# Performance work log

Measured on AMD Instinct MI355X. Metric: run time of the kernel, lower is better.

The kernel has to match this reference:

```python
import jax, jax.numpy as jnp
import numpy as np

N = 8192
DIM_IN = 256
DIM_Q = 64
DIM_K = 64
E = 262144


def setup_inputs() -> dict:
    key = jax.random.key(0)
    ks = jax.random.split(key, 8)
    x = jax.random.normal(ks[0], (N, DIM_IN), dtype=jnp.float32)
    edge_index = jax.random.randint(ks[1], (2, E), 0, N, dtype=jnp.int64)
    s_in = 1.0 / np.sqrt(DIM_IN)
    Wq = jax.random.normal(ks[2], (DIM_IN, DIM_Q), dtype=jnp.float32) * s_in
    bq = jnp.zeros((DIM_Q,), dtype=jnp.float32)
    Wk = jax.random.normal(ks[3], (DIM_IN, DIM_K), dtype=jnp.float32) * s_in
    bk = jnp.zeros((DIM_K,), dtype=jnp.float32)
    Wv = jax.random.normal(ks[4], (DIM_IN, DIM_K), dtype=jnp.float32) * s_in
    bv = jnp.zeros((DIM_K,), dtype=jnp.float32)
    return {"x": x, "edge_index": edge_index, "Wq": Wq, "bq": bq,
            "Wk": Wk, "bk": bk, "Wv": Wv, "bv": bv}


def reference(x, edge_index, Wq, bq, Wk, bk, Wv, bv):
    # q/k/v projections (Dense layers)
    q = x @ Wq + bq            # (N, dim_q)
    k = x @ Wk + bk            # (N, dim_k)
    v = x @ Wv + bv            # (N, dim_k)
    n = x.shape[0]
    # scatter-built dense adjacency, as in the original module
    adj = jnp.zeros((n, n), dtype=x.dtype).at[edge_index[0], edge_index[1]].set(1.0)
    scale = 1.0 / jnp.sqrt(jnp.asarray(q.shape[-1], dtype=x.dtype))
    a = (q @ k.T) * scale      # (N, N)
    a = a * adj + (1.0 - adj) * (-1000000.0)
    attn = jax.nn.softmax(a, axis=-1)
    return attn @ v            # (N, dim_k)
```

## Files before the change

### kernel.cpp

```cpp
#include <hip/hip_runtime.h>
#include <hip/hip_bf16.h>

#define NROW 8192
#define DIM_IN 256
#define DIMK 64
#define NDIM 192
#define NEDGE 262144
#define CAP 128

using bf16 = __hip_bfloat16;
typedef _Float16 f16;
typedef _Float16 f16x8 __attribute__((ext_vector_type(8)));
typedef _Float16 f16x4 __attribute__((ext_vector_type(4)));
typedef float f32x4 __attribute__((ext_vector_type(4)));
typedef unsigned short u16x8 __attribute__((ext_vector_type(8)));

__device__ __forceinline__ float b2f(bf16 x) { return __bfloat162float(x); }
__device__ __forceinline__ float us2f(unsigned short u) {
    return __uint_as_float(((unsigned)u) << 16);
}
__device__ __forceinline__ void wave_sync() {
    asm volatile("s_waitcnt lgkmcnt(0)" ::: "memory");
    __builtin_amdgcn_sched_barrier(0);
}

__device__ __forceinline__ int probe_isb(const unsigned short* xw, int lane) {
    int ex = (xw[lane] >> 7) & 0xFF;
    unsigned long long b = __ballot(ex >= 100 && ex <= 140);
    return (__popcll(b) >= 56) ? 1 : 0;
}
__device__ __forceinline__ int probe_is64(const int* ei, int lane) {
    unsigned long long b = __ballot(ei[2 * lane + 1] != 0);
    return (b == 0ULL) ? 1 : 0;
}
__device__ __forceinline__ int src_at(const int* p, int e, int is64) {
    return is64 ? p[2 * e] : p[e];
}
__device__ __forceinline__ int dst_at(const int* p, int e, int is64) {
    return is64 ? p[2 * (NEDGE + e)] : p[NEDGE + e];
}

__device__ __forceinline__ f16x8 ldcvt(const void* x, size_t off, int isb) {
    f16x8 r;
    if (isb) {
        u16x8 u = *(const u16x8*)((const unsigned short*)x + off);
        #pragma unroll
        for (int i = 0; i < 8; ++i) r[i] = (f16)us2f(u[i]);
    } else {
        float4 f0 = *(const float4*)((const float*)x + off);
        float4 f1 = *(const float4*)((const float*)x + off + 4);
        r[0] = (f16)f0.x; r[1] = (f16)f0.y; r[2] = (f16)f0.z; r[3] = (f16)f0.w;
        r[4] = (f16)f1.x; r[5] = (f16)f1.y; r[6] = (f16)f1.z; r[7] = (f16)f1.w;
    }
    return r;
}

__device__ __forceinline__ void proj_tile16(
    const void* x, const f16* wt, const void* bq, const void* bk,
    const void* bv, int isb, int r0, int wave, int lane,
    f16* qh, f16* kh, f16* vh)
{
    int n0 = wave * 48;
    int lr = lane & 15;
    int lk = (lane >> 4) * 8;

    f32x4 acc0 = {0.f, 0.f, 0.f, 0.f}, acc1 = acc0, acc2 = acc0;
    size_t abase = (size_t)(r0 + lr) * DIM_IN + lk;
    const f16* bp = wt + (size_t)(n0 + lr) * DIM_IN + lk;

    #pragma unroll
    for (int ks = 0; ks < 8; ++ks) {
        f16x8 a  = ldcvt(x, abase + ks * 32, isb);
        f16x8 b0 = *(const f16x8*)(bp + ks * 32);
        f16x8 b1 = *(const f16x8*)(bp + 16 * DIM_IN + ks * 32);
        f16x8 b2 = *(const f16x8*)(bp + 32 * DIM_IN + ks * 32);
        acc0 = __builtin_amdgcn_mfma_f32_16x16x32_f16(a, b0, acc0, 0, 0, 0);
        acc1 = __builtin_amdgcn_mfma_f32_16x16x32_f16(a, b1, acc1, 0, 0, 0);
        acc2 = __builtin_amdgcn_mfma_f32_16x16x32_f16(a, b2, acc2, 0, 0, 0);
    }

    #pragma unroll
    for (int tt = 0; tt < 3; ++tt) {
        f32x4 a = (tt == 0) ? acc0 : (tt == 1) ? acc1 : acc2;
        int d = n0 + tt * 16 + lr;
        int mat = d >> 6, dd = d & 63;
        const void* bb = (mat == 0) ? bq : (mat == 1) ? bk : bv;
        float bias = isb ? b2f(((const bf16*)bb)[dd]) : ((const float*)bb)[dd];
        f16* o = (mat == 0) ? qh : (mat == 1) ? kh : vh;
        #pragma unroll
        for (int j = 0; j < 4; ++j) {
            int r = r0 + (lane >> 4) * 4 + j;
            o[(size_t)r * DIMK + dd] = (f16)(a[j] + bias);
        }
    }
}

__device__ __forceinline__ void attn_row(
    const f16* qh, const f16* kh, const f16* vh, const int* cursor,
    const unsigned short* bucket, float* out, int row, int lane,
    unsigned* bm, unsigned short* nb, float* sc)
{
    *(uint4*)(bm + 4 * lane) = make_uint4(0u, 0u, 0u, 0u);
    wave_sync();

    int deg = cursor[row];
    if (deg > CAP) deg = CAP;
    const unsigned short* bk_ = bucket + (size_t)row * CAP;
    for (int e = lane; e < deg; e += 64) {
        int j = bk_[e];
        atomicOr(&bm[j >> 5], 1u << (j & 31));
    }
    wave_sync();

    uint4 wv = *(const uint4*)(bm + 4 * lane);
    int pc = __popc(wv.x) + __popc(wv.y) + __popc(wv.z) + __popc(wv.w);
    int incl = pc;
    #pragma unroll
    for (int o = 1; o < 64; o <<= 1) {
        int n = __shfl_up(incl, o);
        if (lane >= o) incl += n;
    }
    int nn = __shfl(incl, 63);
    int idx = incl - pc;
    unsigned wrds[4] = {wv.x, wv.y, wv.z, wv.w};
    #pragma unroll
    for (int wi = 0; wi < 4; ++wi) {
        unsigned wb = wrds[wi];
        int boff = 128 * lane + 32 * wi;
        while (wb) {
            int b = __ffs(wb) - 1;
            wb &= wb - 1;
            nb[idx++] = (unsigned short)(boff + b);
        }
    }
    wave_sync();

    if (nn == 0) {
        out[(size_t)row * DIMK + lane] = 0.f;
        return;
    }

    int g = lane >> 4, gl = lane & 15;
    f16x4 qh4 = *(const f16x4*)(qh + (size_t)row * DIMK + 4 * gl);
    float q0 = (float)qh4.x, q1 = (float)qh4.y,
          q2 = (float)qh4.z, q3 = (float)qh4.w;
    for (int i = g; i < nn; i += 4) {
        int j = nb[i];
        f16x4 kk = *(const f16x4*)(kh + (size_t)j * DIMK + 4 * gl);
        float d = q0 * (float)kk.x + q1 * (float)kk.y
                + q2 * (float)kk.z + q3 * (float)kk.w;
        #pragma unroll
        for (int o = 1; o < 16; o <<= 1) d += __shfl_xor(d, o);
        if (gl == 0) sc[i] = d * 0.125f;
    }
    wave_sync();

    float s0 = (lane < nn) ? sc[lane] : -INFINITY;
    float s1 = (lane + 64 < nn) ? sc[lane + 64] : -INFINITY;
    float mx = fmaxf(s0, s1);
    #pragma unroll
    for (int o = 1; o < 64; o <<= 1) mx = fmaxf(mx, __shfl_xor(mx, o));
    float w0 = (lane < nn) ? __expf(s0 - mx) : 0.f;
    float w1 = (lane + 64 < nn) ? __expf(s1 - mx) : 0.f;
    if (lane < nn) sc[lane] = w0;
    if (lane + 64 < nn) sc[lane + 64] = w1;
    float sm = w0 + w1;
    #pragma unroll
    for (int o = 1; o < 64; o <<= 1) sm += __shfl_xor(sm, o);
    wave_sync();

    float acc = 0.f;
    int i = 0;
    for (; i + 4 <= nn; i += 4) {
        int j0 = nb[i], j1 = nb[i + 1], j2 = nb[i + 2], j3 = nb[i + 3];
        float v0 = (float)vh[(size_t)j0 * DIMK + lane];
        float v1 = (float)vh[(size_t)j1 * DIMK + lane];
        float v2 = (float)vh[(size_t)j2 * DIMK + lane];
        float v3 = (float)vh[(size_t)j3 * DIMK + lane];
        acc = fmaf(sc[i], v0, acc);
        acc = fmaf(sc[i + 1], v1, acc);
        acc = fmaf(sc[i + 2], v2, acc);
        acc = fmaf(sc[i + 3], v3, acc);
    }
    for (; i < nn; ++i)
        acc = fmaf(sc[i], (float)vh[(size_t)nb[i] * DIMK + lane], acc);

    out[(size_t)row * DIMK + lane] = acc / sm;
}

__global__ __launch_bounds__(256) void prep_kernel(
    const void* __restrict__ x,
    const void* __restrict__ Wq, const void* __restrict__ Wk,
    const void* __restrict__ Wv,
    f16* __restrict__ wt, int* __restrict__ cursor)
{
    int t = threadIdx.x, lane = t & 63;
    int gid = blockIdx.x * 256 + t;
    if (gid < NROW) cursor[gid] = 0;
    int wi = gid - NROW;
    if (wi >= 0 && wi < NDIM * DIM_IN) {
        int isb = probe_isb((const unsigned short*)x, lane);
        int d = wi >> 8, c = wi & 255;
        int mat = d >> 6, dd = d & 63;
        const void* W = (mat == 0) ? Wq : (mat == 1) ? Wk : Wv;
        float val = isb ? b2f(((const bf16*)W)[c * DIMK + dd])
                        : ((const float*)W)[c * DIMK + dd];
        wt[d * DIM_IN + c] = (f16)val;
    }
}

__global__ __launch_bounds__(256) void proj_scatter_kernel(
    const void* __restrict__ x, const f16* __restrict__ wt,
    const void* __restrict__ bq, const void* __restrict__ bk,
    const void* __restrict__ bv, const int* __restrict__ ei,
    int* __restrict__ cursor, unsigned short* __restrict__ bucket,
    f16* __restrict__ qh, f16* __restrict__ kh, f16* __restrict__ vh)
{
    int t = threadIdx.x, lane = t & 63, wave = t >> 6;
    int isb = probe_isb((const unsigned short*)x, lane);
    int is64 = probe_is64(ei, lane);
    int e0 = blockIdx.x * 512 + t;
    #pragma unroll
    for (int ii = 0; ii < 2; ++ii) {
        int e = e0 + ii * 256;
        int r = src_at(ei, e, is64) & (NROW - 1);
        int c = dst_at(ei, e, is64) & (NROW - 1);
        int pos = atomicAdd(&cursor[r], 1);
        if (pos < CAP) bucket[(size_t)r * CAP + pos] = (unsigned short)c;
    }
    proj_tile16(x, wt, bq, bk, bv, isb, blockIdx.x * 16, wave, lane,
                qh, kh, vh);
}

__global__ __launch_bounds__(256) void attn_kernel(
    const f16* __restrict__ qh, const f16* __restrict__ kh,
    const f16* __restrict__ vh, const int* __restrict__ cursor,
    const unsigned short* __restrict__ bucket, float* __restrict__ out)
{
    __shared__ unsigned bm_all[4][NROW / 32];
    __shared__ unsigned short nb_all[4][CAP];
    __shared__ float sc_all[4][CAP];
    int t = threadIdx.x, lane = t & 63, wave = t >> 6;
    int row = blockIdx.x * 4 + wave;
    attn_row(qh, kh, vh, cursor, bucket, out, row, lane,
             bm_all[wave], nb_all[wave], sc_all[wave]);
}

extern "C" void kernel_launch(void* const* d_in, const int* in_sizes, int n_in,
                              void* d_out, int out_size, void* d_ws, size_t ws_size,
                              hipStream_t stream)
{
    const void* x  = d_in[0];
    const int*  ei = (const int*)d_in[1];
    const void* Wq = d_in[2];
    const void* bq = d_in[3];
    const void* Wk = d_in[4];
    const void* bk = d_in[5];
    const void* Wv = d_in[6];
    const void* bv = d_in[7];
    float* out = (float*)d_out;

    char* W8 = (char*)d_ws;
    f16* wt = (f16*)W8;
    f16* qh = (f16*)(W8 + 98304);
    f16* kh = qh + (size_t)NROW * DIMK;
    f16* vh = kh + (size_t)NROW * DIMK;
    int* cursor = (int*)(vh + (size_t)NROW * DIMK);
    unsigned short* bucket = (unsigned short*)(cursor + NROW);
    size_t need = (size_t)((char*)(bucket + (size_t)NROW * CAP) - W8);
    if (ws_size < need) return;

    prep_kernel<<<224, 256, 0, stream>>>(x, Wq, Wk, Wv, wt, cursor);
    proj_scatter_kernel<<<512, 256, 0, stream>>>(x, wt, bq, bk, bv, ei,
                                                 cursor, bucket, qh, kh, vh);
    attn_kernel<<<2048, 256, 0, stream>>>(qh, kh, vh, cursor, bucket, out);
}
```

Measured before the change: 47.41 us.

## Deduplicate edges with a global bitmap during scatter and interleave K/V storage

Edge deduplication moves from a per-row shared-memory bitmap in the attention kernel to a global 8 MB N×N bitmap. The scatter kernel atomically ORs into that bitmap and appends only first-seen columns to the bucket. The attention kernel then drops the bitmap clear, the prefix scan and the bit extraction, and copies the bucket straight into shared memory. K and V are interleaved into one 128-wide row, the score loop handles two neighbours per iteration, the V accumulation uses two accumulators, and launch bounds request higher occupancy. The cost is clearing 8 MB of bitmap in the prep kernel every call. Neighbour order is now nondeterministic, which changes summation order.

```diff
diff --git a/kernel.cpp b/kernel.cpp
--- a/kernel.cpp
+++ b/kernel.cpp
@@ -6,6 +6,7 @@
 #define DIMK 64
 #define NDIM 192
 #define NEDGE 262144
+#define NBW (NROW / 32)
 #define CAP 128
 
 using bf16 = __hip_bfloat16;
@@ -55,12 +56,54 @@
     return r;
 }
 
-__device__ __forceinline__ void proj_tile16(
-    const void* x, const f16* wt, const void* bq, const void* bk,
-    const void* bv, int isb, int r0, int wave, int lane,
-    f16* qh, f16* kh, f16* vh)
-{
+__global__ __launch_bounds__(256) void prep_kernel(
+    const void* __restrict__ x,
+    const void* __restrict__ Wq, const void* __restrict__ Wk,
+    const void* __restrict__ Wv,
+    f16* __restrict__ wt, int* __restrict__ cursor, unsigned* __restrict__ gbm)
+{
+    int t = threadIdx.x, lane = t & 63;
+    int i = blockIdx.x * 256 + t;
+    ((uint4*)gbm)[i] = make_uint4(0u, 0u, 0u, 0u);
+    if (i < NROW) cursor[i] = 0;
+    if (blockIdx.x < NDIM) {
+        int isb = probe_isb((const unsigned short*)x, lane);
+        int d = blockIdx.x, c = t;
+        int mat = d >> 6, dd = d & 63;
+        const void* W = (mat == 0) ? Wq : (mat == 1) ? Wk : Wv;
+        float val = isb ? b2f(((const bf16*)W)[c * DIMK + dd])
+                        : ((const float*)W)[c * DIMK + dd];
+        wt[d * DIM_IN + c] = (f16)val;
+    }
+}
+
+__global__ __launch_bounds__(256) void proj_scatter_kernel(
+    const void* __restrict__ x, const f16* __restrict__ wt,
+    const void* __restrict__ bq, const void* __restrict__ bk,
+    const void* __restrict__ bv, const int* __restrict__ ei,
+    unsigned* __restrict__ gbm, int* __restrict__ cursor,
+    unsigned short* __restrict__ bucket,
+    f16* __restrict__ qh, f16* __restrict__ kv)
+{
+    int t = threadIdx.x, lane = t & 63, wave = t >> 6;
+    int isb = probe_isb((const unsigned short*)x, lane);
+    int is64 = probe_is64(ei, lane);
+
+    #pragma unroll
+    for (int ii = 0; ii < 2; ++ii) {
+        int e = blockIdx.x * 512 + t + ii * 256;
+        int r = src_at(ei, e, is64) & (NROW - 1);
+        int c = dst_at(ei, e, is64) & (NROW - 1);
+        unsigned bit = 1u << (c & 31);
+        unsigned old = atomicOr(&gbm[r * NBW + (c >> 5)], bit);
+        if (!(old & bit)) {
+            int pos = atomicAdd(&cursor[r], 1);
+            if (pos < CAP) bucket[(size_t)r * CAP + pos] = (unsigned short)c;
+        }
+    }
+
     int n0 = wave * 48;
+    int r0 = blockIdx.x * 16;
     int lr = lane & 15;
     int lk = (lane >> 4) * 8;
 
@@ -86,53 +129,34 @@
         int mat = d >> 6, dd = d & 63;
         const void* bb = (mat == 0) ? bq : (mat == 1) ? bk : bv;
         float bias = isb ? b2f(((const bf16*)bb)[dd]) : ((const float*)bb)[dd];
-        f16* o = (mat == 0) ? qh : (mat == 1) ? kh : vh;
         #pragma unroll
         for (int j = 0; j < 4; ++j) {
             int r = r0 + (lane >> 4) * 4 + j;
-            o[(size_t)r * DIMK + dd] = (f16)(a[j] + bias);
-        }
-    }
-}
-
-__device__ __forceinline__ void attn_row(
-    const f16* qh, const f16* kh, const f16* vh, const int* cursor,
-    const unsigned short* bucket, float* out, int row, int lane,
-    unsigned* bm, unsigned short* nb, float* sc)
-{
-    *(uint4*)(bm + 4 * lane) = make_uint4(0u, 0u, 0u, 0u);
-    wave_sync();
-
-    int deg = cursor[row];
-    if (deg > CAP) deg = CAP;
+            float val = a[j] + bias;
+            if (mat == 0)      qh[(size_t)r * DIMK + dd] = (f16)val;
+            else if (mat == 1) kv[(size_t)r * 128 + dd] = (f16)val;
+            else               kv[(size_t)r * 128 + 64 + dd] = (f16)val;
+        }
+    }
+}
+
+__global__ __launch_bounds__(256, 8) void attn_kernel(
+    const f16* __restrict__ qh, const f16* __restrict__ kv,
+    const int* __restrict__ cursor, const unsigned short* __restrict__ bucket,
+    float* __restrict__ out)
+{
+    __shared__ unsigned short nb_all[4][CAP];
+    __shared__ float sc_all[4][CAP];
+    int t = threadIdx.x, lane = t & 63, wave = t >> 6;
+    int row = blockIdx.x * 4 + wave;
+    unsigned short* nb = nb_all[wave];
+    float* sc = sc_all[wave];
+
+    int nn = cursor[row];
+    if (nn > CAP) nn = CAP;
     const unsigned short* bk_ = bucket + (size_t)row * CAP;
-    for (int e = lane; e < deg; e += 64) {
-        int j = bk_[e];
-        atomicOr(&bm[j >> 5], 1u << (j & 31));
-    }
-    wave_sync();
-
-    uint4 wv = *(const uint4*)(bm + 4 * lane);
-    int pc = __popc(wv.x) + __popc(wv.y) + __popc(wv.z) + __popc(wv.w);
-    int incl = pc;
-    #pragma unroll
-    for (int o = 1; o < 64; o <<= 1) {
-        int n = __shfl_up(incl, o);
-        if (lane >= o) incl += n;
-    }
-    int nn = __shfl(incl, 63);
-    int idx = incl - pc;
-    unsigned wrds[4] = {wv.x, wv.y, wv.z, wv.w};
-    #pragma unroll
-    for (int wi = 0; wi < 4; ++wi) {
-        unsigned wb = wrds[wi];
-        int boff = 128 * lane + 32 * wi;
-        while (wb) {
-            int b = __ffs(wb) - 1;
-            wb &= wb - 1;
-            nb[idx++] = (unsigned short)(boff + b);
-        }
-    }
+    if (lane < nn) nb[lane] = bk_[lane];
+    if (lane + 64 < nn) nb[lane + 64] = bk_[lane + 64];
     wave_sync();
 
     if (nn == 0) {
@@ -144,14 +168,25 @@
     f16x4 qh4 = *(const f16x4*)(qh + (size_t)row * DIMK + 4 * gl);
     float q0 = (float)qh4.x, q1 = (float)qh4.y,
           q2 = (float)qh4.z, q3 = (float)qh4.w;
-    for (int i = g; i < nn; i += 4) {
-        int j = nb[i];
-        f16x4 kk = *(const f16x4*)(kh + (size_t)j * DIMK + 4 * gl);
-        float d = q0 * (float)kk.x + q1 * (float)kk.y
-                + q2 * (float)kk.z + q3 * (float)kk.w;
+    for (int i = 0; i < nn; i += 8) {
+        int ia = i + g, ib = i + 4 + g;
+        int ja = (ia < nn) ? nb[ia] : 0;
+        int jb = (ib < nn) ? nb[ib] : 0;
+        f16x4 ka = *(const f16x4*)(kv + (size_t)ja * 128 + 4 * gl);
+        f16x4 kb2 = *(const f16x4*)(kv + (size_t)jb * 128 + 4 * gl);
+        float da = q0 * (float)ka.x + q1 * (float)ka.y
+                 + q2 * (float)ka.z + q3 * (float)ka.w;
+        float db = q0 * (float)kb2.x + q1 * (float)kb2.y
+                 + q2 * (float)kb2.z + q3 * (float)kb2.w;
         #pragma unroll
-        for (int o = 1; o < 16; o <<= 1) d += __shfl_xor(d, o);
-        if (gl == 0) sc[i] = d * 0.125f;
+        for (int o = 1; o < 16; o <<= 1) {
+            da += __shfl_xor(da, o);
+            db += __shfl_xor(db, o);
+        }
+        if (gl == 0) {
+            if (ia < nn) sc[ia] = da * 0.125f;
+            if (ib < nn) sc[ib] = db * 0.125f;
+        }
     }
     wave_sync();
 
@@ -169,81 +204,23 @@
     for (int o = 1; o < 64; o <<= 1) sm += __shfl_xor(sm, o);
     wave_sync();
 
-    float acc = 0.f;
+    float acca = 0.f, accb = 0.f;
     int i = 0;
     for (; i + 4 <= nn; i += 4) {
         int j0 = nb[i], j1 = nb[i + 1], j2 = nb[i + 2], j3 = nb[i + 3];
-        float v0 = (float)vh[(size_t)j0 * DIMK + lane];
-        float v1 = (float)vh[(size_t)j1 * DIMK + lane];
-        float v2 = (float)vh[(size_t)j2 * DIMK + lane];
-        float v3 = (float)vh[(size_t)j3 * DIMK + lane];
-        acc = fmaf(sc[i], v0, acc);
-        acc = fmaf(sc[i + 1], v1, acc);
-        acc = fmaf(sc[i + 2], v2, acc);
-        acc = fmaf(sc[i + 3], v3, acc);
+        float v0 = (float)kv[(size_t)j0 * 128 + 64 + lane];
+        float v1 = (float)kv[(size_t)j1 * 128 + 64 + lane];
+        float v2 = (float)kv[(size_t)j2 * 128 + 64 + lane];
+        float v3 = (float)kv[(size_t)j3 * 128 + 64 + lane];
+        acca = fmaf(sc[i], v0, acca);
+        accb = fmaf(sc[i + 1], v1, accb);
+        acca = fmaf(sc[i + 2], v2, acca);
+        accb = fmaf(sc[i + 3], v3, accb);
     }
     for (; i < nn; ++i)
-        acc = fmaf(sc[i], (float)vh[(size_t)nb[i] * DIMK + lane], acc);
-
-    out[(size_t)row * DIMK + lane] = acc / sm;
-}
-
-__global__ __launch_bounds__(256) void prep_kernel(
-    const void* __restrict__ x,
-    const void* __restrict__ Wq, const void* __restrict__ Wk,
-    const void* __restrict__ Wv,
-    f16* __restrict__ wt, int* __restrict__ cursor)
-{
-    int t = threadIdx.x, lane = t & 63;
-    int gid = blockIdx.x * 256 + t;
-    if (gid < NROW) cursor[gid] = 0;
-    int wi = gid - NROW;
-    if (wi >= 0 && wi < NDIM * DIM_IN) {
-        int isb = probe_isb((const unsigned short*)x, lane);
-        int d = wi >> 8, c = wi & 255;
-        int mat = d >> 6, dd = d & 63;
-        const void* W = (mat == 0) ? Wq : (mat == 1) ? Wk : Wv;
-        float val = isb ? b2f(((const bf16*)W)[c * DIMK + dd])
-                        : ((const float*)W)[c * DIMK + dd];
-        wt[d * DIM_IN + c] = (f16)val;
-    }
-}
-
-__global__ __launch_bounds__(256) void proj_scatter_kernel(
-    const void* __restrict__ x, const f16* __restrict__ wt,
-    const void* __restrict__ bq, const void* __restrict__ bk,
-    const void* __restrict__ bv, const int* __restrict__ ei,
-    int* __restrict__ cursor, unsigned short* __restrict__ bucket,
-    f16* __restrict__ qh, f16* __restrict__ kh, f16* __restrict__ vh)
-{
-    int t = threadIdx.x, lane = t & 63, wave = t >> 6;
-    int isb = probe_isb((const unsigned short*)x, lane);
-    int is64 = probe_is64(ei, lane);
-    int e0 = blockIdx.x * 512 + t;
-    #pragma unroll
-    for (int ii = 0; ii < 2; ++ii) {
-        int e = e0 + ii * 256;
-        int r = src_at(ei, e, is64) & (NROW - 1);
-        int c = dst_at(ei, e, is64) & (NROW - 1);
-        int pos = atomicAdd(&cursor[r], 1);
-        if (pos < CAP) bucket[(size_t)r * CAP + pos] = (unsigned short)c;
-    }
-    proj_tile16(x, wt, bq, bk, bv, isb, blockIdx.x * 16, wave, lane,
-                qh, kh, vh);
-}
-
-__global__ __launch_bounds__(256) void attn_kernel(
-    const f16* __restrict__ qh, const f16* __restrict__ kh,
-    const f16* __restrict__ vh, const int* __restrict__ cursor,
-    const unsigned short* __restrict__ bucket, float* __restrict__ out)
-{
-    __shared__ unsigned bm_all[4][NROW / 32];
-    __shared__ unsigned short nb_all[4][CAP];
-    __shared__ float sc_all[4][CAP];
-    int t = threadIdx.x, lane = t & 63, wave = t >> 6;
-    int row = blockIdx.x * 4 + wave;
-    attn_row(qh, kh, vh, cursor, bucket, out, row, lane,
-             bm_all[wave], nb_all[wave], sc_all[wave]);
+        acca = fmaf(sc[i], (float)kv[(size_t)nb[i] * 128 + 64 + lane], acca);
+
+    out[(size_t)row * DIMK + lane] = (acca + accb) / sm;
 }
 
 extern "C" void kernel_launch(void* const* d_in, const int* in_sizes, int n_in,
@@ -261,17 +238,17 @@
     float* out = (float*)d_out;
 
     char* W8 = (char*)d_ws;
-    f16* wt = (f16*)W8;
-    f16* qh = (f16*)(W8 + 98304);
-    f16* kh = qh + (size_t)NROW * DIMK;
-    f16* vh = kh + (size_t)NROW * DIMK;
-    int* cursor = (int*)(vh + (size_t)NROW * DIMK);
+    unsigned* gbm = (unsigned*)W8;
+    f16* wt = (f16*)(W8 + (size_t)8 * 1024 * 1024);
+    f16* qh = (f16*)(W8 + (size_t)8 * 1024 * 1024 + 98304);
+    f16* kv = qh + (size_t)NROW * DIMK;
+    int* cursor = (int*)(kv + (size_t)NROW * 128);
     unsigned short* bucket = (unsigned short*)(cursor + NROW);
     size_t need = (size_t)((char*)(bucket + (size_t)NROW * CAP) - W8);
     if (ws_size < need) return;
 
-    prep_kernel<<<224, 256, 0, stream>>>(x, Wq, Wk, Wv, wt, cursor);
+    prep_kernel<<<2048, 256, 0, stream>>>(x, Wq, Wk, Wv, wt, cursor, gbm);
     proj_scatter_kernel<<<512, 256, 0, stream>>>(x, wt, bq, bk, bv, ei,
-                                                 cursor, bucket, qh, kh, vh);
-    attn_kernel<<<2048, 256, 0, stream>>>(qh, kh, vh, cursor, bucket, out);
-}
+                                                 gbm, cursor, bucket, qh, kv);
+    attn_kernel<<<2048, 256, 0, stream>>>(qh, kv, cursor, bucket, out);
+}
```

New measurement: 57.69 us. +21.7%, slower.
